# Optimization experiments

Hardware: AMD Instinct MI355X
Metric: run time of the kernel (lower is better)

Reference implementation:

```python
import jax, jax.numpy as jnp
import numpy as np
import math

HIDDEN = 1024
HEADS = 16
D_K = HIDDEN // HEADS
EPS = 1e-5


def gelu_tanh(x):
    c = math.sqrt(2.0 / math.pi)
    return 0.5 * x * (1.0 + jnp.tanh(c * (x + 0.044715 * x ** 3)))


def layer_norm(x, gamma, beta):
    mu = jnp.mean(x, axis=-1, keepdims=True)
    var = jnp.mean((x - mu) ** 2, axis=-1, keepdims=True)
    return (x - mu) * jax.lax.rsqrt(var + EPS) * gamma + beta


def setup_inputs() -> dict:
    key = jax.random.key(0)
    ks = jax.random.split(key, 12)
    s = 1.0 / math.sqrt(HIDDEN)
    s4 = 1.0 / math.sqrt(4 * HIDDEN)
    inp = {
        "x": jax.random.normal(ks[0], (2, 2048, HIDDEN), dtype=jnp.float32),
        # attention linears, stored as (in, out) so y = x @ W + b
        "Wq": jax.random.uniform(ks[1], (HIDDEN, HIDDEN), minval=-s, maxval=s),
        "bq": jax.random.uniform(ks[2], (HIDDEN,), minval=-s, maxval=s),
        "Wv": jax.random.uniform(ks[3], (HIDDEN, HIDDEN), minval=-s, maxval=s),
        "bv": jax.random.uniform(ks[4], (HIDDEN,), minval=-s, maxval=s),
        "Wo": jax.random.uniform(ks[5], (HIDDEN, HIDDEN), minval=-s, maxval=s),
        "bo": jax.random.uniform(ks[6], (HIDDEN,), minval=-s, maxval=s),
        # feed-forward
        "W1": jax.random.uniform(ks[7], (HIDDEN, 4 * HIDDEN), minval=-s, maxval=s),
        "b1": jax.random.uniform(ks[8], (4 * HIDDEN,), minval=-s, maxval=s),
        "W2": jax.random.uniform(ks[9], (4 * HIDDEN, HIDDEN), minval=-s4, maxval=s4),
        "b2": jax.random.uniform(ks[10], (HIDDEN,), minval=-s4, maxval=s4),
        # layer norms
        "g1": jnp.ones((HIDDEN,), jnp.float32),
        "beta1": jnp.zeros((HIDDEN,), jnp.float32),
        "g2": jnp.ones((HIDDEN,), jnp.float32),
        "beta2": jnp.zeros((HIDDEN,), jnp.float32),
    }
    return inp


def attention(x, Wq, bq, Wv, bv, Wo, bo):
    bs, seq, _ = x.shape
    qk = (x @ Wq + bq).reshape(bs, seq, HEADS, D_K).transpose(0, 2, 1, 3)  # b h s d
    v = (x @ Wv + bv).reshape(bs, seq, HEADS, D_K).transpose(0, 2, 1, 3)
    scores = jnp.einsum('bhqd,bhkd->bhqk', qk, qk) / math.sqrt(D_K)
    causal = jnp.tril(jnp.ones((seq, seq), dtype=bool))
    scores = jnp.where(causal[None, None], scores, -jnp.inf)
    attn = jax.nn.softmax(scores, axis=-1)
    out = jnp.einsum('bhqk,bhkd->bhqd', attn, v)
    out = out.transpose(0, 2, 1, 3).reshape(bs, seq, HIDDEN)
    return out @ Wo + bo


def reference(x, Wq, bq, Wv, bv, Wo, bo, W1, b1, W2, b2, g1, beta1, g2, beta2):
    x = x + attention(layer_norm(x, g1, beta1), Wq, bq, Wv, bv, Wo, bo)
    h = layer_norm(x, g2, beta2)
    ff = gelu_tanh(h @ W1 + b1) @ W2 + b2  # chunking is a memory detail; same math
    return x + ff
```

## Files before the change

kernel.cpp:

```cpp
#include <hip/hip_runtime.h>

typedef unsigned short u16;
typedef short bf16x8 __attribute__((ext_vector_type(8)));
typedef float f32x4 __attribute__((ext_vector_type(4)));

__device__ __forceinline__ float bf2f(u16 u) {
    union { unsigned int i; float f; } v; v.i = ((unsigned int)u) << 16; return v.f;
}
__device__ __forceinline__ u16 f2bf(float f) {
    union { float f; unsigned int i; } v; v.f = f;
    unsigned int r = v.i + 0x7fffu + ((v.i >> 16) & 1u);
    return (u16)(r >> 16);
}
__device__ __forceinline__ float gelu(float u) {
    float y = 0.7978845608028654f * (u + 0.044715f * u * u * u);
    float t = __expf(2.0f * y);
    return 0.5f * u * (1.0f + (1.0f - 2.0f / (t + 1.0f)));
}

__device__ __forceinline__ void gload16(const u16* g, u16* l) {
    __builtin_amdgcn_global_load_lds((__attribute__((address_space(1))) void*)(u16*)g,
                                     (__attribute__((address_space(3))) void*)l, 16, 0, 0);
}

__global__ __launch_bounds__(256) void prep(const float* __restrict__ Wq,
                                            const float* __restrict__ Wv,
                                            const float* __restrict__ Wo,
                                            const float* __restrict__ W1,
                                            const float* __restrict__ W2,
                                            const float* __restrict__ bq,
                                            const float* __restrict__ bv,
                                            const float* __restrict__ x,
                                            const float* __restrict__ g1,
                                            const float* __restrict__ be1,
                                            u16* __restrict__ WqT, u16* __restrict__ WvT,
                                            u16* __restrict__ WoT, u16* __restrict__ W1T,
                                            u16* __restrict__ W2T, float* __restrict__ bqv,
                                            u16* __restrict__ h1) {
    int id = blockIdx.x;
    int tid = threadIdx.x;
    if (id >= 2824) {
        int row = id - 2824;
        int lane = tid & 63, wave = tid >> 6;
        float4 f4 = *(const float4*)(x + (size_t)row * 1024 + tid * 4);
        float v[4] = {f4.x, f4.y, f4.z, f4.w};
        float s1 = v[0] + v[1] + v[2] + v[3];
        float s2 = v[0]*v[0] + v[1]*v[1] + v[2]*v[2] + v[3]*v[3];
#pragma unroll
        for (int mm = 1; mm < 64; mm <<= 1) { s1 += __shfl_xor(s1, mm); s2 += __shfl_xor(s2, mm); }
        __shared__ float a1[4], a2[4];
        if (lane == 0) { a1[wave] = s1; a2[wave] = s2; }
        __syncthreads();
        s1 = a1[0] + a1[1] + a1[2] + a1[3];
        s2 = a2[0] + a2[1] + a2[2] + a2[3];
        float mean = s1 * (1.0f / 1024.0f);
        float var  = s2 * (1.0f / 1024.0f) - mean * mean;
        float rstd = rsqrtf(var + 1e-5f);
#pragma unroll
        for (int i = 0; i < 4; ++i) {
            int c = tid * 4 + i;
            h1[(size_t)row * 1024 + c] = f2bf((v[i] - mean) * rstd * g1[c] + be1[c]);
        }
        return;
    }
    if (id >= 2816) {
        int i = (id - 2816) * 256 + tid;
        bqv[i] = (i < 1024) ? bq[i] : bv[i - 1024];
        return;
    }
    const float* in; u16* out; int R, C, bx, by;
    if (id < 256)       { in = Wq; out = WqT; R = 1024; C = 1024; bx = id & 15;          by = id >> 4; }
    else if (id < 512)  { int t = id - 256;  in = Wv; out = WvT; R = 1024; C = 1024; bx = t & 15; by = t >> 4; }
    else if (id < 768)  { int t = id - 512;  in = Wo; out = WoT; R = 1024; C = 1024; bx = t & 15; by = t >> 4; }
    else if (id < 1792) { int t = id - 768;  in = W1; out = W1T; R = 1024; C = 4096; bx = t & 63; by = t >> 6; }
    else                { int t = id - 1792; in = W2; out = W2T; R = 4096; C = 1024; bx = t & 15; by = t >> 4; }
    __shared__ u16 tile[64][65];
    int c0 = bx * 64, r0 = by * 64;
    for (int i = tid; i < 4096; i += 256) {
        int r = i >> 6, c = i & 63;
        tile[r][c] = f2bf(in[(size_t)(r0 + r) * C + c0 + c]);
    }
    __syncthreads();
    for (int i = tid; i < 4096; i += 256) {
        int r = i >> 6, c = i & 63;
        out[(size_t)(c0 + r) * R + r0 + c] = tile[c][r];
    }
}

__global__ __launch_bounds__(256) void transpose_bf16_s(const u16* __restrict__ in,
                                                        u16* __restrict__ out,
                                                        int R, int C, int istride) {
    __shared__ u16 tile[64][65];
    int c0 = blockIdx.x * 64, r0 = blockIdx.y * 64;
    in  += (size_t)blockIdx.z * R * istride;
    out += (size_t)blockIdx.z * R * C;
    for (int i = threadIdx.x; i < 4096; i += 256) {
        int r = i >> 6, c = i & 63;
        tile[r][c] = in[(size_t)(r0 + r) * istride + c0 + c];
    }
    __syncthreads();
    for (int i = threadIdx.x; i < 4096; i += 256) {
        int r = i >> 6, c = i & 63;
        out[(size_t)(c0 + r) * R + r0 + c] = tile[c][r];
    }
}

__global__ __launch_bounds__(256) void ln_bf16(const u16* __restrict__ x,
                                               const float* __restrict__ g,
                                               const float* __restrict__ be,
                                               u16* __restrict__ out) {
    int row = blockIdx.x, tid = threadIdx.x;
    int lane = tid & 63, wave = tid >> 6;
    u16 e[4]; *(uint2*)e = *(const uint2*)(x + (size_t)row * 1024 + tid * 4);
    float v[4];
#pragma unroll
    for (int i = 0; i < 4; ++i) v[i] = bf2f(e[i]);
    float s1 = v[0] + v[1] + v[2] + v[3];
    float s2 = v[0]*v[0] + v[1]*v[1] + v[2]*v[2] + v[3]*v[3];
#pragma unroll
    for (int mm = 1; mm < 64; mm <<= 1) { s1 += __shfl_xor(s1, mm); s2 += __shfl_xor(s2, mm); }
    __shared__ float a1[4], a2[4];
    if (lane == 0) { a1[wave] = s1; a2[wave] = s2; }
    __syncthreads();
    s1 = a1[0] + a1[1] + a1[2] + a1[3];
    s2 = a2[0] + a2[1] + a2[2] + a2[3];
    float mean = s1 * (1.0f / 1024.0f);
    float var  = s2 * (1.0f / 1024.0f) - mean * mean;
    float rstd = rsqrtf(var + 1e-5f);
#pragma unroll
    for (int i = 0; i < 4; ++i) {
        int c = tid * 4 + i;
        out[(size_t)row * 1024 + c] = f2bf((v[i] - mean) * rstd * g[c] + be[c]);
    }
}

template <int BN, int ACT, int RES>
__global__ __launch_bounds__(256) void gemm_gl(const u16* __restrict__ A,
                                               const u16* __restrict__ WT,
                                               const float* __restrict__ bias,
                                               const float* __restrict__ resid,
                                               u16* __restrict__ C,
                                               int M, int N, int K, int cpx) {
    constexpr int JN = BN / 32;
    constexpr int TS = BN + 8;
    __shared__ u16 lds_a[128 * 64];
    __shared__ u16 lds_b[BN * 64];
    int tid = threadIdx.x;
    int lane = tid & 63, wave = tid >> 6;
    int l16 = lane & 15, quad = lane >> 4;
    int wm = (wave >> 1) * 64, wn = (wave & 1) * (BN / 2);

    int id = blockIdx.x;
    int slot = id >> 3;
    int bx = (id & 7) * cpx + (slot >> 5);
    int by = slot & 31;
    int m0 = by * 128, n0 = bx * BN;
    f32x4 acc[4][JN] = {};

    int scol = ((lane & 7) ^ (lane >> 3)) * 8;
    const u16* Ab = A  + (size_t)(m0 + wave * 8 + (lane >> 3)) * K + scol;
    const u16* Bb = WT + (size_t)(n0 + wave * 8 + (lane >> 3)) * K + scol;
    u16* la = lds_a + wave * 512;
    u16* lb = lds_b + wave * 512;
    int xk = (l16 & 7);

    for (int k0 = 0; k0 < K; k0 += 64) {
        __syncthreads();
#pragma unroll
        for (int it = 0; it < 4; ++it)
            gload16(Ab + (size_t)it * 32 * K + k0, la + it * 2048);
#pragma unroll
        for (int it = 0; it < JN; ++it)
            gload16(Bb + (size_t)it * 32 * K + k0, lb + it * 2048);
        __syncthreads();
#pragma unroll
        for (int s = 0; s < 2; ++s) {
            bf16x8 af[4], bfr[JN];
#pragma unroll
            for (int i = 0; i < 4; ++i)
                af[i] = *(const bf16x8*)&lds_a[(wm + i * 16 + l16) * 64 + (((s * 4 + quad) ^ xk) * 8)];
#pragma unroll
            for (int j = 0; j < JN; ++j)
                bfr[j] = *(const bf16x8*)&lds_b[(wn + j * 16 + l16) * 64 + (((s * 4 + quad) ^ xk) * 8)];
#pragma unroll
            for (int i = 0; i < 4; ++i)
#pragma unroll
                for (int j = 0; j < JN; ++j)
                    acc[i][j] = __builtin_amdgcn_mfma_f32_16x16x32_bf16(af[i], bfr[j], acc[i][j], 0, 0, 0);
        }
    }

    u16* et = lds_a;
    int erow = tid >> 3;
    int lr0  = (wave >> 1) * 16 + quad * 4;
    float bvj[JN];
#pragma unroll
    for (int j = 0; j < JN; ++j) bvj[j] = bias[n0 + wn + j * 16 + l16];
#pragma unroll
    for (int i = 0; i < 4; ++i) {
        __syncthreads();
#pragma unroll
        for (int j = 0; j < JN; ++j) {
            int col = wn + j * 16 + l16;
#pragma unroll
            for (int r = 0; r < 4; ++r) {
                float v = acc[i][j][r] + bvj[j];
                if (ACT) v = gelu(v);
                if (RES) v += resid[(size_t)(m0 + wm + i * 16 + quad * 4 + r) * N + n0 + col];
                et[(lr0 + r) * TS + col] = f2bf(v);
            }
        }
        __syncthreads();
        int grow = m0 + (erow >> 4) * 64 + i * 16 + (erow & 15);
        if (BN == 128) {
            int ec = (tid & 7) * 16;
            uint4 d0 = *(const uint4*)&et[erow * TS + ec];
            uint4 d1 = *(const uint4*)&et[erow * TS + ec + 8];
            *(uint4*)&C[(size_t)grow * N + n0 + ec]     = d0;
            *(uint4*)&C[(size_t)grow * N + n0 + ec + 8] = d1;
        } else {
            int ec = (tid & 7) * 8;
            uint4 d0 = *(const uint4*)&et[erow * TS + ec];
            *(uint4*)&C[(size_t)grow * N + n0 + ec] = d0;
        }
    }
}

template <int ACT>
__global__ __launch_bounds__(256, 3) void gemm_big(const u16* __restrict__ A,
                                                   const u16* __restrict__ WT,
                                                   const float* __restrict__ bias,
                                                   u16* __restrict__ C,
                                                   int M, int N, int K) {
    __shared__ u16 lds_a[256 * 64];
    __shared__ u16 lds_b[128 * 64];
    int tid = threadIdx.x;
    int lane = tid & 63, wave = tid >> 6;
    int l16 = lane & 15, quad = lane >> 4;
    int wm = (wave >> 1) * 128, wn = (wave & 1) * 64;
    int id = blockIdx.x;
    int bx = id & 31, by = id >> 5;
    int m0 = by * 256, n0 = bx * 128;
    f32x4 acc[8][4] = {};

    int scol = ((lane & 7) ^ (lane >> 3)) * 8;
    const u16* Ab = A  + (size_t)(m0 + wave * 8 + (lane >> 3)) * K + scol;
    const u16* Bb = WT + (size_t)(n0 + wave * 8 + (lane >> 3)) * K + scol;
    u16* la = lds_a + wave * 512;
    u16* lb = lds_b + wave * 512;
    int xk = (l16 & 7);

    for (int k0 = 0; k0 < K; k0 += 64) {
        __syncthreads();
#pragma unroll
        for (int it = 0; it < 8; ++it)
            gload16(Ab + (size_t)it * 32 * K + k0, la + it * 2048);
#pragma unroll
        for (int it = 0; it < 4; ++it)
            gload16(Bb + (size_t)it * 32 * K + k0, lb + it * 2048);
        __syncthreads();
#pragma unroll
        for (int s = 0; s < 2; ++s) {
            bf16x8 bfr[4];
#pragma unroll
            for (int j = 0; j < 4; ++j)
                bfr[j] = *(const bf16x8*)&lds_b[(wn + j * 16 + l16) * 64 + (((s * 4 + quad) ^ xk) * 8)];
#pragma unroll
            for (int i = 0; i < 8; ++i) {
                bf16x8 af = *(const bf16x8*)&lds_a[(wm + i * 16 + l16) * 64 + (((s * 4 + quad) ^ xk) * 8)];
#pragma unroll
                for (int j = 0; j < 4; ++j)
                    acc[i][j] = __builtin_amdgcn_mfma_f32_16x16x32_bf16(af, bfr[j], acc[i][j], 0, 0, 0);
            }
        }
    }

    constexpr int TS = 136;
    u16* et = lds_a;
    int erow = tid >> 3;
    int ec   = (tid & 7) * 16;
    int lr0  = (wave >> 1) * 16 + quad * 4;
    float bvj[4];
#pragma unroll
    for (int j = 0; j < 4; ++j) bvj[j] = bias[n0 + wn + j * 16 + l16];
#pragma unroll
    for (int i = 0; i < 8; ++i) {
        __syncthreads();
#pragma unroll
        for (int j = 0; j < 4; ++j) {
            int col = wn + j * 16 + l16;
#pragma unroll
            for (int r = 0; r < 4; ++r) {
                float v = acc[i][j][r] + bvj[j];
                if (ACT) v = gelu(v);
                et[(lr0 + r) * TS + col] = f2bf(v);
            }
        }
        __syncthreads();
        int grow = m0 + (erow >> 4) * 128 + i * 16 + (erow & 15);
        uint4 d0 = *(const uint4*)&et[erow * TS + ec];
        uint4 d1 = *(const uint4*)&et[erow * TS + ec + 8];
        *(uint4*)&C[(size_t)grow * N + n0 + ec]     = d0;
        *(uint4*)&C[(size_t)grow * N + n0 + ec + 8] = d1;
    }
}

__global__ __launch_bounds__(256, 3) void gemm_split(const u16* __restrict__ A,
                                                     const u16* __restrict__ WT,
                                                     u16* __restrict__ p0,
                                                     u16* __restrict__ p1,
                                                     u16* __restrict__ p2,
                                                     int M, int N, int K) {
    __shared__ u16 lds_a[256 * 64];
    __shared__ u16 lds_b[128 * 64];
    int tid = threadIdx.x;
    int lane = tid & 63, wave = tid >> 6;
    int l16 = lane & 15, quad = lane >> 4;
    int wm = (wave >> 1) * 128, wn = (wave & 1) * 64;
    int id = blockIdx.x;
    int u = id >> 3;
    int by = (id & 7) * 2 + (u & 1);
    int bx = (u >> 1) & 7;
    int slice = u >> 4;
    int m0 = by * 256, n0 = bx * 128;
    int k_lo = (slice == 0) ? 0 : 64 * (22 + 21 * (slice - 1));
    int k_hi = (slice == 2) ? K : 64 * (22 + 21 * slice);
    u16* P = (slice == 0) ? p0 : (slice == 1) ? p1 : p2;
    f32x4 acc[8][4] = {};

    int scol = ((lane & 7) ^ (lane >> 3)) * 8;
    const u16* Ab = A  + (size_t)(m0 + wave * 8 + (lane >> 3)) * K + scol;
    const u16* Bb = WT + (size_t)(n0 + wave * 8 + (lane >> 3)) * K + scol;
    u16* la = lds_a + wave * 512;
    u16* lb = lds_b + wave * 512;
    int xk = (l16 & 7);

    for (int k0 = k_lo; k0 < k_hi; k0 += 64) {
        __syncthreads();
#pragma unroll
        for (int it = 0; it < 8; ++it)
            gload16(Ab + (size_t)it * 32 * K + k0, la + it * 2048);
#pragma unroll
        for (int it = 0; it < 4; ++it)
            gload16(Bb + (size_t)it * 32 * K + k0, lb + it * 2048);
        __syncthreads();
#pragma unroll
        for (int s = 0; s < 2; ++s) {
            bf16x8 bfr[4];
#pragma unroll
            for (int j = 0; j < 4; ++j)
                bfr[j] = *(const bf16x8*)&lds_b[(wn + j * 16 + l16) * 64 + (((s * 4 + quad) ^ xk) * 8)];
#pragma unroll
            for (int i = 0; i < 8; ++i) {
                bf16x8 af = *(const bf16x8*)&lds_a[(wm + i * 16 + l16) * 64 + (((s * 4 + quad) ^ xk) * 8)];
#pragma unroll
                for (int j = 0; j < 4; ++j)
                    acc[i][j] = __builtin_amdgcn_mfma_f32_16x16x32_bf16(af, bfr[j], acc[i][j], 0, 0, 0);
            }
        }
    }

    constexpr int TS = 136;
    u16* et = lds_a;
    int erow = tid >> 3;
    int ec   = (tid & 7) * 16;
    int lr0  = (wave >> 1) * 16 + quad * 4;
#pragma unroll
    for (int i = 0; i < 8; ++i) {
        __syncthreads();
#pragma unroll
        for (int j = 0; j < 4; ++j) {
            int col = wn + j * 16 + l16;
#pragma unroll
            for (int r = 0; r < 4; ++r)
                et[(lr0 + r) * TS + col] = f2bf(acc[i][j][r]);
        }
        __syncthreads();
        int grow = m0 + (erow >> 4) * 128 + i * 16 + (erow & 15);
        uint4 d0 = *(const uint4*)&et[erow * TS + ec];
        uint4 d1 = *(const uint4*)&et[erow * TS + ec + 8];
        *(uint4*)&P[(size_t)grow * N + n0 + ec]     = d0;
        *(uint4*)&P[(size_t)grow * N + n0 + ec + 8] = d1;
    }
}

__global__ __launch_bounds__(256) void ff2_reduce(const u16* __restrict__ p0,
                                                  const u16* __restrict__ p1,
                                                  const u16* __restrict__ p2,
                                                  const u16* __restrict__ x2b,
                                                  const float* __restrict__ b2,
                                                  float* __restrict__ out) {
    size_t i = ((size_t)blockIdx.x * 256 + threadIdx.x) * 8;
    int col = (int)(i & 1023);
    uint4 a0 = *(const uint4*)&p0[i];
    uint4 a1 = *(const uint4*)&p1[i];
    uint4 a2 = *(const uint4*)&p2[i];
    uint4 ax = *(const uint4*)&x2b[i];
    const u16* e0 = (const u16*)&a0;
    const u16* e1 = (const u16*)&a1;
    const u16* e2 = (const u16*)&a2;
    const u16* ex = (const u16*)&ax;
    float o[8];
#pragma unroll
    for (int e = 0; e < 8; ++e)
        o[e] = bf2f(ex[e]) + bf2f(e0[e]) + bf2f(e1[e]) + bf2f(e2[e]) + b2[col + e];
    *(float4*)&out[i]     = *(float4*)&o[0];
    *(float4*)&out[i + 4] = *(float4*)&o[4];
}

__global__ __launch_bounds__(256) void attn_kernel(const u16* __restrict__ QV,
                                                   const u16* __restrict__ Vt,
                                                   u16* __restrict__ Out) {
    int id = blockIdx.x;
    int slot = id >> 3;
    int hb = (id & 7) + 8 * (slot & 3);
    int t  = 31 - (slot >> 2);
    int h = hb & 15, b = hb >> 4;
    int tid = threadIdx.x;
    int lane = tid & 63, wave = tid >> 6;
    int l16 = lane & 15, quad = lane >> 4;

    __shared__ u16 k_lds[64 * 64];
    __shared__ u16 v_lds[64 * 64];
    __shared__ u16 p_lds[4][16 * 72];

    bf16x8 ones;
#pragma unroll
    for (int e = 0; e < 8; ++e) ones[e] = (short)0x3F80;

    int srow = wave * 8 + (lane >> 3);
    int sc8  = ((lane & 7) ^ (lane >> 3)) * 8;
    int xk   = (l16 & 7);

    int q0 = t * 64;
    const u16* qp = QV + ((size_t)b * 2048 + q0 + wave * 16 + l16) * 2048 + h * 64;
    bf16x8 qf[2];
    qf[0] = *(const bf16x8*)&qp[quad * 8];
    qf[1] = *(const bf16x8*)&qp[32 + quad * 8];

    f32x4 O[4] = {};
    f32x4 L = {};

    for (int kt = 0; kt <= t; ++kt) {
        const u16* kg = QV + ((size_t)b * 2048 + kt * 64 + srow) * 2048 + h * 64 + sc8;
        const u16* vg = Vt + ((((size_t)b * 16 + h) * 64) + srow) * 2048 + kt * 64 + sc8;
        __syncthreads();
        gload16(kg,                      k_lds + wave * 512);
        gload16(kg + (size_t)32 * 2048,  k_lds + wave * 512 + 2048);
        gload16(vg,                      v_lds + wave * 512);
        gload16(vg + (size_t)32 * 2048,  v_lds + wave * 512 + 2048);
        __syncthreads();

        f32x4 S[4] = {};
#pragma unroll
        for (int s = 0; s < 2; ++s)
#pragma unroll
            for (int j = 0; j < 4; ++j) {
                bf16x8 kf = *(const bf16x8*)&k_lds[(j * 16 + l16) * 64 + (((s * 4 + quad) ^ xk) * 8)];
                S[j] = __builtin_amdgcn_mfma_f32_16x16x32_bf16(qf[s], kf, S[j], 0, 0, 0);
            }

        if (kt == t) {
#pragma unroll
            for (int j = 0; j < 4; ++j) {
                int key = j * 16 + l16;
#pragma unroll
                for (int r = 0; r < 4; ++r)
                    if (key > wave * 16 + quad * 4 + r) S[j][r] = -1e30f;
            }
        }

#pragma unroll
        for (int j = 0; j < 4; ++j)
#pragma unroll
            for (int r = 0; r < 4; ++r) {
                float pp = __expf(S[j][r] * 0.125f);
                p_lds[wave][(quad * 4 + r) * 72 + j * 16 + l16] = f2bf(pp);
            }

#pragma unroll
        for (int s = 0; s < 2; ++s) {
            bf16x8 pf = *(const bf16x8*)&p_lds[wave][l16 * 72 + s * 32 + quad * 8];
            L = __builtin_amdgcn_mfma_f32_16x16x32_bf16(pf, ones, L, 0, 0, 0);
#pragma unroll
            for (int dj = 0; dj < 4; ++dj) {
                bf16x8 vf = *(const bf16x8*)&v_lds[(dj * 16 + l16) * 64 + (((s * 4 + quad) ^ xk) * 8)];
                O[dj] = __builtin_amdgcn_mfma_f32_16x16x32_bf16(pf, vf, O[dj], 0, 0, 0);
            }
        }
    }

#pragma unroll
    for (int r = 0; r < 4; ++r) {
        int qg = q0 + wave * 16 + quad * 4 + r;
        float inv = 1.0f / L[r];
#pragma unroll
        for (int dj = 0; dj < 4; ++dj)
            Out[((size_t)b * 2048 + qg) * 1024 + h * 64 + dj * 16 + l16] =
                f2bf(O[dj][r] * inv);
    }
}

extern "C" void kernel_launch(void* const* d_in, const int* in_sizes, int n_in,
                              void* d_out, int out_size, void* d_ws, size_t ws_size,
                              hipStream_t stream) {
    const float* x   = (const float*)d_in[0];
    const float* Wq  = (const float*)d_in[1];
    const float* bq  = (const float*)d_in[2];
    const float* Wv  = (const float*)d_in[3];
    const float* bv  = (const float*)d_in[4];
    const float* Wo  = (const float*)d_in[5];
    const float* bo  = (const float*)d_in[6];
    const float* W1  = (const float*)d_in[7];
    const float* b1  = (const float*)d_in[8];
    const float* W2  = (const float*)d_in[9];
    const float* b2  = (const float*)d_in[10];
    const float* g1  = (const float*)d_in[11];
    const float* be1 = (const float*)d_in[12];
    const float* g2  = (const float*)d_in[13];
    const float* be2 = (const float*)d_in[14];

    char* ws = (char*)d_ws;
    const size_t MB = 1 << 20;
    u16*   WqT  = (u16*)(ws + 0  * MB);
    u16*   WvT  = (u16*)(ws + 2  * MB);
    u16*   WoT  = (u16*)(ws + 4  * MB);
    u16*   W1T  = (u16*)(ws + 6  * MB);
    u16*   W2T  = (u16*)(ws + 14 * MB);
    u16*   h1   = (u16*)(ws + 22 * MB);
    u16*   QV   = (u16*)(ws + 30 * MB);
    u16*   x2b  = (u16*)(ws + 30 * MB);
    u16*   Vt   = (u16*)(ws + 46 * MB);
    u16*   ff1  = (u16*)(ws + 46 * MB);
    float* bqv  = (float*)(ws + 78 * MB);
    u16*   fp0  = (u16*)(ws + 0  * MB);
    u16*   fp1  = (u16*)(ws + 22 * MB);
    u16*   fp2  = (u16*)(ws + 38 * MB);

    prep<<<6920, 256, 0, stream>>>(Wq, Wv, Wo, W1, W2, bq, bv, x, g1, be1,
                                   WqT, WvT, WoT, W1T, W2T, bqv, h1);

    gemm_gl<128, 0, 0><<<512, 256, 0, stream>>>(h1, WqT, bqv, nullptr, QV, 4096, 2048, 1024, 2);

    transpose_bf16_s<<<dim3(16, 32, 2), 256, 0, stream>>>(QV + 1024, Vt, 2048, 1024, 2048);

    attn_kernel<<<1024, 256, 0, stream>>>(QV, Vt, h1);

    gemm_gl<64, 0, 1><<<512, 256, 0, stream>>>(h1, WoT, bo, x, x2b, 4096, 1024, 1024, 2);

    ln_bf16<<<4096, 256, 0, stream>>>(x2b, g2, be2, h1);

    gemm_big<1><<<512, 256, 0, stream>>>(h1, W1T, b1, ff1, 4096, 4096, 1024);

    gemm_split<<<384, 256, 0, stream>>>(ff1, W2T, fp0, fp1, fp2, 4096, 1024, 4096);

    ff2_reduce<<<2048, 256, 0, stream>>>(fp0, fp1, fp2, x2b, b2, (float*)d_out);
}
```

Measured before the change: 324.7 us.

## Use 128-key attention tiles and remap GEMM block indices by XCD

```diff
diff --git a/kernel.cpp b/kernel.cpp
--- a/kernel.cpp
+++ b/kernel.cpp
@@ -140,7 +140,7 @@
                                                const float* __restrict__ bias,
                                                const float* __restrict__ resid,
                                                u16* __restrict__ C,
-                                               int M, int N, int K, int cpx) {
+                                               int M, int N, int K) {
     constexpr int JN = BN / 32;
     constexpr int TS = BN + 8;
     __shared__ u16 lds_a[128 * 64];
@@ -151,9 +151,9 @@
     int wm = (wave >> 1) * 64, wn = (wave & 1) * (BN / 2);
 
     int id = blockIdx.x;
-    int slot = id >> 3;
-    int bx = (id & 7) * cpx + (slot >> 5);
-    int by = slot & 31;
+    int u = id >> 3;
+    int by = (id & 7) * 4 + (u & 3);
+    int bx = u >> 2;
     int m0 = by * 128, n0 = bx * BN;
     f32x4 acc[4][JN] = {};
 
@@ -239,7 +239,9 @@
     int l16 = lane & 15, quad = lane >> 4;
     int wm = (wave >> 1) * 128, wn = (wave & 1) * 64;
     int id = blockIdx.x;
-    int bx = id & 31, by = id >> 5;
+    int u = id >> 3;
+    int by = (id & 7) * 2 + (u & 1);
+    int bx = u >> 1;
     int m0 = by * 256, n0 = bx * 128;
     f32x4 acc[8][4] = {};
 
@@ -420,17 +422,19 @@
     int lane = tid & 63, wave = tid >> 6;
     int l16 = lane & 15, quad = lane >> 4;
 
-    __shared__ u16 k_lds[64 * 64];
-    __shared__ u16 v_lds[64 * 64];
-    __shared__ u16 p_lds[4][16 * 72];
+    __shared__ u16 k_lds[128 * 64];
+    __shared__ u16 v_lds[64 * 128];
+    __shared__ u16 p_lds[4][16 * 136];
 
     bf16x8 ones;
 #pragma unroll
     for (int e = 0; e < 8; ++e) ones[e] = (short)0x3F80;
 
-    int srow = wave * 8 + (lane >> 3);
-    int sc8  = ((lane & 7) ^ (lane >> 3)) * 8;
-    int xk   = (l16 & 7);
+    int srowK = wave * 8 + (lane >> 3);
+    int scK   = ((lane & 7) ^ (lane >> 3)) * 8;
+    int vrow  = wave * 4 + (lane >> 4);
+    int scV   = ((lane & 15) ^ vrow) * 8;
+    int xk    = (l16 & 7);
 
     int q0 = t * 64;
     const u16* qp = QV + ((size_t)b * 2048 + q0 + wave * 16 + l16) * 2048 + h * 64;
@@ -441,53 +445,59 @@
     f32x4 O[4] = {};
     f32x4 L = {};
 
-    for (int kt = 0; kt <= t; ++kt) {
-        const u16* kg = QV + ((size_t)b * 2048 + kt * 64 + srow) * 2048 + h * 64 + sc8;
-        const u16* vg = Vt + ((((size_t)b * 16 + h) * 64) + srow) * 2048 + kt * 64 + sc8;
-        __syncthreads();
-        gload16(kg,                      k_lds + wave * 512);
-        gload16(kg + (size_t)32 * 2048,  k_lds + wave * 512 + 2048);
-        gload16(vg,                      v_lds + wave * 512);
-        gload16(vg + (size_t)32 * 2048,  v_lds + wave * 512 + 2048);
-        __syncthreads();
-
-        f32x4 S[4] = {};
+    int nsteps = (t >> 1) + 1;
+    for (int kt2 = 0; kt2 < nsteps; ++kt2) {
+        const u16* kg = QV + ((size_t)b * 2048 + kt2 * 128 + srowK) * 2048 + h * 64 + scK;
+        const u16* vg = Vt + ((((size_t)b * 16 + h) * 64) + vrow) * 2048 + kt2 * 128 + scV;
+        __syncthreads();
+#pragma unroll
+        for (int it = 0; it < 4; ++it)
+            gload16(kg + (size_t)it * 32 * 2048, k_lds + wave * 512 + it * 2048);
+#pragma unroll
+        for (int it = 0; it < 4; ++it)
+            gload16(vg + (size_t)it * 16 * 2048, v_lds + wave * 512 + it * 2048);
+        __syncthreads();
+
+        f32x4 S[8] = {};
 #pragma unroll
         for (int s = 0; s < 2; ++s)
 #pragma unroll
-            for (int j = 0; j < 4; ++j) {
+            for (int j = 0; j < 8; ++j) {
                 bf16x8 kf = *(const bf16x8*)&k_lds[(j * 16 + l16) * 64 + (((s * 4 + quad) ^ xk) * 8)];
                 S[j] = __builtin_amdgcn_mfma_f32_16x16x32_bf16(qf[s], kf, S[j], 0, 0, 0);
             }
 
-        if (kt == t) {
-#pragma unroll
-            for (int j = 0; j < 4; ++j) {
-                int key = j * 16 + l16;
+        if (kt2 == nsteps - 1) {
+#pragma unroll
+            for (int j = 0; j < 8; ++j) {
+                int key = kt2 * 128 + j * 16 + l16;
 #pragma unroll
                 for (int r = 0; r < 4; ++r)
-                    if (key > wave * 16 + quad * 4 + r) S[j][r] = -1e30f;
-            }
-        }
-
-#pragma unroll
-        for (int j = 0; j < 4; ++j)
+                    if (key > q0 + wave * 16 + quad * 4 + r) S[j][r] = -1e30f;
+            }
+        }
+
+#pragma unroll
+        for (int j = 0; j < 8; ++j)
 #pragma unroll
             for (int r = 0; r < 4; ++r) {
                 float pp = __expf(S[j][r] * 0.125f);
-                p_lds[wave][(quad * 4 + r) * 72 + j * 16 + l16] = f2bf(pp);
-            }
-
-#pragma unroll
-        for (int s = 0; s < 2; ++s) {
-            bf16x8 pf = *(const bf16x8*)&p_lds[wave][l16 * 72 + s * 32 + quad * 8];
-            L = __builtin_amdgcn_mfma_f32_16x16x32_bf16(pf, ones, L, 0, 0, 0);
-#pragma unroll
-            for (int dj = 0; dj < 4; ++dj) {
-                bf16x8 vf = *(const bf16x8*)&v_lds[(dj * 16 + l16) * 64 + (((s * 4 + quad) ^ xk) * 8)];
-                O[dj] = __builtin_amdgcn_mfma_f32_16x16x32_bf16(pf, vf, O[dj], 0, 0, 0);
-            }
-        }
+                p_lds[wave][(quad * 4 + r) * 136 + j * 16 + l16] = f2bf(pp);
+            }
+
+#pragma unroll
+        for (int ktt = 0; ktt < 2; ++ktt)
+#pragma unroll
+            for (int s = 0; s < 2; ++s) {
+                bf16x8 pf = *(const bf16x8*)&p_lds[wave][l16 * 136 + ktt * 64 + s * 32 + quad * 8];
+                L = __builtin_amdgcn_mfma_f32_16x16x32_bf16(pf, ones, L, 0, 0, 0);
+                int c = ktt * 8 + s * 4 + quad;
+#pragma unroll
+                for (int dj = 0; dj < 4; ++dj) {
+                    bf16x8 vfr = *(const bf16x8*)&v_lds[(dj * 16 + l16) * 128 + ((c ^ l16) * 8)];
+                    O[dj] = __builtin_amdgcn_mfma_f32_16x16x32_bf16(pf, vfr, O[dj], 0, 0, 0);
+                }
+            }
     }
 
 #pragma unroll
@@ -540,13 +550,13 @@
     prep<<<6920, 256, 0, stream>>>(Wq, Wv, Wo, W1, W2, bq, bv, x, g1, be1,
                                    WqT, WvT, WoT, W1T, W2T, bqv, h1);
 
-    gemm_gl<128, 0, 0><<<512, 256, 0, stream>>>(h1, WqT, bqv, nullptr, QV, 4096, 2048, 1024, 2);
+    gemm_gl<128, 0, 0><<<512, 256, 0, stream>>>(h1, WqT, bqv, nullptr, QV, 4096, 2048, 1024);
 
     transpose_bf16_s<<<dim3(16, 32, 2), 256, 0, stream>>>(QV + 1024, Vt, 2048, 1024, 2048);
 
     attn_kernel<<<1024, 256, 0, stream>>>(QV, Vt, h1);
 
-    gemm_gl<64, 0, 1><<<512, 256, 0, stream>>>(h1, WoT, bo, x, x2b, 4096, 1024, 1024, 2);
+    gemm_gl<64, 0, 1><<<512, 256, 0, stream>>>(h1, WoT, bo, x, x2b, 4096, 1024, 1024);
 
     ln_bf16<<<4096, 256, 0, stream>>>(x2b, g2, be2, h1);
 
```

After: 314.2 us. 3.2% less time.
